# Optimization experiments

Measured on AMD Instinct MI355X. Metric: run time of the kernel, lower is better.

## Reference

```python
import jax, jax.numpy as jnp
import numpy as np

WINDOW = 512          # init window_size
OVERLAP = WINDOW // 4 # 128
FADE = OVERLAP // 2   # 64
ROPE_BASE = 10000.0


def _rope(x, pos):
    # x: (B,H,nw,W,D), pos: (nw,W) float
    D = x.shape[-1]
    inv_freq = 1.0 / (ROPE_BASE ** (jnp.arange(0, D, 2, dtype=jnp.float32) / D))
    ang = pos[..., None] * inv_freq                     # (nw,W,D/2)
    cos = jnp.concatenate([jnp.cos(ang), jnp.cos(ang)], -1)[None, None]  # (1,1,nw,W,D)
    sin = jnp.concatenate([jnp.sin(ang), jnp.sin(ang)], -1)[None, None]
    x1, x2 = x[..., : D // 2], x[..., D // 2 :]
    rot = jnp.concatenate([-x2, x1], -1)
    return x * cos + rot * sin


def setup_inputs() -> dict:
    key = jax.random.key(0)
    k1, k2, k3 = jax.random.split(key, 3)
    B, H, L, D = 2, 16, 8192, 64
    return {
        "query": jax.random.normal(k1, (B, H, L, D), jnp.float32),
        "key": jax.random.normal(k2, (B, H, L, D), jnp.float32),
        "value": jax.random.normal(k3, (B, H, L, D), jnp.float32),
        "position_ids": jnp.arange(L, dtype=jnp.int64),
    }


def reference(query, key, value, position_ids):
    B, H, L, D = query.shape
    nw = L // WINDOW
    qw = query.reshape(B, H, nw, WINDOW, D)
    kw = key.reshape(B, H, nw, WINDOW, D)
    vw = value.reshape(B, H, nw, WINDOW, D)
    pos = position_ids.reshape(nw, WINDOW).astype(jnp.float32)

    q = _rope(qw, pos)
    k = _rope(kw, pos)

    scores = jnp.einsum("bhnqd,bhnkd->bhnqk", q, k) / jnp.sqrt(jnp.float32(D))
    attn = jax.nn.softmax(scores, axis=-1)
    win_out = jnp.einsum("bhnqk,bhnkd->bhnqd", attn, vw)  # (B,H,nw,W,D)

    # overlap-fade blend weights per window (middle windows fade at edges;
    # first/last windows use full weight). out = win_out * w / (w + 1e-8).
    fade_in = jnp.linspace(0.0, 1.0, FADE)
    fade_out = jnp.linspace(1.0, 0.0, FADE)
    w_mid = jnp.concatenate([fade_in, jnp.ones(WINDOW - 2 * FADE), fade_out])
    w_edge = jnp.ones(WINDOW)
    idx = jnp.arange(nw)
    is_edge = (idx == 0) | (idx == nw - 1)
    w = jnp.where(is_edge[:, None], w_edge[None, :], w_mid[None, :])  # (nw,W)
    scale = (w / (w + 1e-8))[None, None, :, :, None]
    out = win_out * scale
    return out.reshape(B, H, L, D)
```

## Files before the change

kernel.cpp:

```cpp
#include <hip/hip_runtime.h>

typedef _Float16 half8 __attribute__((ext_vector_type(8)));
typedef _Float16 half4 __attribute__((ext_vector_type(4)));
typedef _Float16 half2v __attribute__((ext_vector_type(2)));
typedef float floatx4 __attribute__((ext_vector_type(4)));
typedef float floatx2 __attribute__((ext_vector_type(2)));

#define MFMA_F16 __builtin_amdgcn_mfma_f32_16x16x32_f16
#define FREQ (-0.41524101186092f)

__global__ __launch_bounds__(512, 4) void swa4(
    const float* __restrict__ Q, const float* __restrict__ K,
    const float* __restrict__ V, const int* __restrict__ pid,
    float* __restrict__ Out)
{
    __shared__ __align__(16) _Float16 lq[128 * 72];
    __shared__ __align__(16) _Float16 lk[2][32 * 64];
    __shared__ __align__(16) _Float16 lvt[2][64 * 32];
    __shared__ __align__(16) _Float16 lp[8][16 * 40];

    const int bid   = blockIdx.x;
    const int half_ = (bid >> 3) & 1;
    const int win   = (bid & 7) | ((bid >> 4) << 3);
    const int n = win & 15, bh = win >> 4;
    const long long winrow = (long long)bh * 8192 + n * 512;
    const long long qbase  = winrow + half_ * 256;
    const float* Qb = Q + qbase * 64;
    const float* Kb = K + winrow * 64;
    const float* Vb = V + winrow * 64;
    float* Ob = Out + qbase * 64;
    const int pidq = n * 512 + half_ * 256;
    const int pidk = n * 512;

    const int tid = threadIdx.x, lane = tid & 63, wv = tid >> 6;
    const int l15 = lane & 15, quad = (lane >> 4) & 3;
    const float CS = 0.125f * 1.44269504088896f;

    half8 qf[2][2];
    {
        const int rowl = tid >> 2;
        const int dq   = (tid & 3) * 8;
        float ifq[8];
        #pragma unroll
        for (int i = 0; i < 8; ++i) ifq[i] = __builtin_exp2f((float)(dq + i) * FREQ);
        for (int rnd = 0; rnd < 2; ++rnd) {
            const float* src = Qb + (rnd * 128 + rowl) * 64;
            float pos = (float)pid[pidq + rnd * 128 + rowl];
            float4 a0 = *(const float4*)(src + dq);
            float4 a1 = *(const float4*)(src + dq + 4);
            float4 b0 = *(const float4*)(src + 32 + dq);
            float4 b1 = *(const float4*)(src + 36 + dq);
            float lo[8] = {a0.x,a0.y,a0.z,a0.w,a1.x,a1.y,a1.z,a1.w};
            float hi[8] = {b0.x,b0.y,b0.z,b0.w,b1.x,b1.y,b1.z,b1.w};
            half8 wlo, whi;
            #pragma unroll
            for (int i = 0; i < 8; ++i) {
                float sn, cn;
                __sincosf(pos * ifq[i], &sn, &cn);
                wlo[i] = (_Float16)((lo[i] * cn - hi[i] * sn) * CS);
                whi[i] = (_Float16)((hi[i] * cn + lo[i] * sn) * CS);
            }
            if (rnd) __syncthreads();
            *(half8*)&lq[rowl * 72 + dq]      = wlo;
            *(half8*)&lq[rowl * 72 + 32 + dq] = whi;
            __syncthreads();
            if ((wv >> 2) == rnd) {
                const int rb = (wv & 3) * 32;
                #pragma unroll
                for (int rt = 0; rt < 2; ++rt) {
                    qf[rt][0] = *(const half8*)&lq[(rb + rt * 16 + l15) * 72 + quad * 8];
                    qf[rt][1] = *(const half8*)&lq[(rb + rt * 16 + l15) * 72 + 32 + quad * 8];
                }
            }
        }
    }

    floatx4 o[2][4], ol[2];
    #pragma unroll
    for (int rt = 0; rt < 2; ++rt) {
        ol[rt] = (floatx4){0.f, 0.f, 0.f, 0.f};
        #pragma unroll
        for (int vt = 0; vt < 4; ++vt) o[rt][vt] = (floatx4){0.f, 0.f, 0.f, 0.f};
    }
    half8 onesf;
    #pragma unroll
    for (int i = 0; i < 8; ++i) onesf[i] = (_Float16)1.0f;

    const int key = tid >> 4;
    const int pr  = tid & 15;
    const int dv  = tid & 63;
    const int grp = tid >> 6;
    float if2[2];
    #pragma unroll
    for (int i = 0; i < 2; ++i) if2[i] = __builtin_exp2f((float)(pr * 2 + i) * FREQ);
    const int klo_addr = key * 64 + (((pr >> 2) ^ (key & 7)) * 8) + (pr & 3) * 2;
    const int khi_addr = key * 64 + ((((pr >> 2) + 4) ^ (key & 7)) * 8) + (pr & 3) * 2;
    const int vst_addr = dv * 32 + (((grp >> 1) ^ ((dv >> 1) & 3)) * 8) + (grp & 1) * 4;
    const int ksw0 = (quad ^ (l15 & 7)) * 8;
    const int ksw1 = ((quad + 4) ^ (l15 & 7)) * 8;
    const int vsw  = (quad ^ ((l15 >> 1) & 3)) * 8;

    floatx2 ka  = *(const floatx2*)(Kb + key * 64 + pr * 2);
    floatx2 kb2 = *(const floatx2*)(Kb + key * 64 + 32 + pr * 2);
    float vr[4];
    #pragma unroll
    for (int i = 0; i < 4; ++i) vr[i] = Vb[(grp * 4 + i) * 64 + dv];
    int kp = pid[pidk + key];

    for (int kc = 0; kc < 16; ++kc) {
        const int cur = kc & 1;
        float kpos = (float)kp;
        half2v klo, khi;
        {
            float a[2] = {ka.x, ka.y};
            float b[2] = {kb2.x, kb2.y};
            #pragma unroll
            for (int i = 0; i < 2; ++i) {
                float sn, cn;
                __sincosf(kpos * if2[i], &sn, &cn);
                klo[i] = (_Float16)(a[i] * cn - b[i] * sn);
                khi[i] = (_Float16)(b[i] * cn + a[i] * sn);
            }
        }
        half4 vh;
        #pragma unroll
        for (int i = 0; i < 4; ++i) vh[i] = (_Float16)vr[i];

        *(half2v*)&lk[cur][klo_addr] = klo;
        *(half2v*)&lk[cur][khi_addr] = khi;
        *(half4*)&lvt[cur][vst_addr] = vh;
        __syncthreads();

        if (kc < 15) {
            const float* kn = Kb + (kc + 1) * 2048;
            const float* vn = Vb + (kc + 1) * 2048;
            ka  = *(const floatx2*)(kn + key * 64 + pr * 2);
            kb2 = *(const floatx2*)(kn + key * 64 + 32 + pr * 2);
            #pragma unroll
            for (int i = 0; i < 4; ++i) vr[i] = vn[(grp * 4 + i) * 64 + dv];
            kp = pid[pidk + (kc + 1) * 32 + key];
        }

        half8 kf00 = *(const half8*)&lk[cur][l15 * 64 + ksw0];
        half8 kf01 = *(const half8*)&lk[cur][l15 * 64 + ksw1];
        half8 kf10 = *(const half8*)&lk[cur][(16 + l15) * 64 + ksw0];
        half8 kf11 = *(const half8*)&lk[cur][(16 + l15) * 64 + ksw1];
        half8 vf[4];
        #pragma unroll
        for (int vt = 0; vt < 4; ++vt)
            vf[vt] = *(const half8*)&lvt[cur][(vt * 16 + l15) * 32 + vsw];

        #pragma unroll
        for (int rt = 0; rt < 2; ++rt) {
            floatx4 s0 = {0.f,0.f,0.f,0.f}, s1 = {0.f,0.f,0.f,0.f};
            s0 = MFMA_F16(qf[rt][0], kf00, s0, 0, 0, 0);
            s0 = MFMA_F16(qf[rt][1], kf01, s0, 0, 0, 0);
            s1 = MFMA_F16(qf[rt][0], kf10, s1, 0, 0, 0);
            s1 = MFMA_F16(qf[rt][1], kf11, s1, 0, 0, 0);

            #pragma unroll
            for (int r = 0; r < 4; ++r) {
                float p0 = __builtin_exp2f(s0[r]);
                float p1 = __builtin_exp2f(s1[r]);
                lp[wv][(quad * 4 + r) * 40 + l15]      = (_Float16)p0;
                lp[wv][(quad * 4 + r) * 40 + 16 + l15] = (_Float16)p1;
            }
            half8 pf = *(const half8*)&lp[wv][l15 * 40 + quad * 8];
            ol[rt] = MFMA_F16(pf, onesf, ol[rt], 0, 0, 0);
            #pragma unroll
            for (int vt = 0; vt < 4; ++vt)
                o[rt][vt] = MFMA_F16(pf, vf[vt], o[rt][vt], 0, 0, 0);
        }
    }

    #pragma unroll
    for (int rt = 0; rt < 2; ++rt) {
        #pragma unroll
        for (int r = 0; r < 4; ++r) {
            int rowl = wv * 32 + rt * 16 + quad * 4 + r;
            int j = half_ * 256 + rowl;
            float w;
            if (n == 0 || n == 15)  w = 1.0f;
            else if (j < 64)        w = (float)j * (1.0f / 63.0f);
            else if (j >= 448)      w = (float)(511 - j) * (1.0f / 63.0f);
            else                    w = 1.0f;
            float f = (w / (w + 1e-8f)) / ol[rt][r];
            #pragma unroll
            for (int vt = 0; vt < 4; ++vt)
                Ob[rowl * 64 + vt * 16 + l15] = o[rt][vt][r] * f;
        }
    }
}

extern "C" void kernel_launch(void* const* d_in, const int* in_sizes, int n_in,
                              void* d_out, int out_size, void* d_ws, size_t ws_size,
                              hipStream_t stream) {
    const float* q   = (const float*)d_in[0];
    const float* k   = (const float*)d_in[1];
    const float* v   = (const float*)d_in[2];
    const int*   pid = (const int*)d_in[3];
    float* out = (float*)d_out;
    (void)in_sizes; (void)n_in; (void)out_size; (void)d_ws; (void)ws_size;
    swa4<<<dim3(1024), dim3(512), 0, stream>>>(q, k, v, pid, out);
}
```

Baseline: 238.1 us.

## Compute transposed scores so P stays in registers, drop LDS P round-trip

```diff
diff --git a/kernel.cpp b/kernel.cpp
--- a/kernel.cpp
+++ b/kernel.cpp
@@ -9,7 +9,12 @@
 #define MFMA_F16 __builtin_amdgcn_mfma_f32_16x16x32_f16
 #define FREQ (-0.41524101186092f)
 
-__global__ __launch_bounds__(512, 4) void swa4(
+static __device__ __forceinline__ unsigned pack_f16(float a, float b) {
+    half2v h; h.x = (_Float16)a; h.y = (_Float16)b;
+    return __builtin_bit_cast(unsigned, h);
+}
+
+__global__ __launch_bounds__(512, 4) void swa6(
     const float* __restrict__ Q, const float* __restrict__ K,
     const float* __restrict__ V, const int* __restrict__ pid,
     float* __restrict__ Out)
@@ -17,7 +22,6 @@
     __shared__ __align__(16) _Float16 lq[128 * 72];
     __shared__ __align__(16) _Float16 lk[2][32 * 64];
     __shared__ __align__(16) _Float16 lvt[2][64 * 32];
-    __shared__ __align__(16) _Float16 lp[8][16 * 40];
 
     const int bid   = blockIdx.x;
     const int half_ = (bid >> 3) & 1;
@@ -95,7 +99,7 @@
     for (int i = 0; i < 2; ++i) if2[i] = __builtin_exp2f((float)(pr * 2 + i) * FREQ);
     const int klo_addr = key * 64 + (((pr >> 2) ^ (key & 7)) * 8) + (pr & 3) * 2;
     const int khi_addr = key * 64 + ((((pr >> 2) + 4) ^ (key & 7)) * 8) + (pr & 3) * 2;
-    const int vst_addr = dv * 32 + (((grp >> 1) ^ ((dv >> 1) & 3)) * 8) + (grp & 1) * 4;
+    const int vst_addr = dv * 32 + (((grp & 3) ^ ((dv >> 1) & 3)) * 8) + (grp >> 2) * 4;
     const int ksw0 = (quad ^ (l15 & 7)) * 8;
     const int ksw1 = ((quad + 4) ^ (l15 & 7)) * 8;
     const int vsw  = (quad ^ ((l15 >> 1) & 3)) * 8;
@@ -150,27 +154,28 @@
         for (int vt = 0; vt < 4; ++vt)
             vf[vt] = *(const half8*)&lvt[cur][(vt * 16 + l15) * 32 + vsw];
 
+        __builtin_amdgcn_s_setprio(1);
         #pragma unroll
         for (int rt = 0; rt < 2; ++rt) {
             floatx4 s0 = {0.f,0.f,0.f,0.f}, s1 = {0.f,0.f,0.f,0.f};
-            s0 = MFMA_F16(qf[rt][0], kf00, s0, 0, 0, 0);
-            s0 = MFMA_F16(qf[rt][1], kf01, s0, 0, 0, 0);
-            s1 = MFMA_F16(qf[rt][0], kf10, s1, 0, 0, 0);
-            s1 = MFMA_F16(qf[rt][1], kf11, s1, 0, 0, 0);
-
-            #pragma unroll
-            for (int r = 0; r < 4; ++r) {
-                float p0 = __builtin_exp2f(s0[r]);
-                float p1 = __builtin_exp2f(s1[r]);
-                lp[wv][(quad * 4 + r) * 40 + l15]      = (_Float16)p0;
-                lp[wv][(quad * 4 + r) * 40 + 16 + l15] = (_Float16)p1;
-            }
-            half8 pf = *(const half8*)&lp[wv][l15 * 40 + quad * 8];
+            s0 = MFMA_F16(kf00, qf[rt][0], s0, 0, 0, 0);
+            s0 = MFMA_F16(kf01, qf[rt][1], s0, 0, 0, 0);
+            s1 = MFMA_F16(kf10, qf[rt][0], s1, 0, 0, 0);
+            s1 = MFMA_F16(kf11, qf[rt][1], s1, 0, 0, 0);
+
+            union { unsigned u[4]; half8 h; } pfu;
+            pfu.u[0] = pack_f16(__builtin_exp2f(s0[0]), __builtin_exp2f(s0[1]));
+            pfu.u[1] = pack_f16(__builtin_exp2f(s0[2]), __builtin_exp2f(s0[3]));
+            pfu.u[2] = pack_f16(__builtin_exp2f(s1[0]), __builtin_exp2f(s1[1]));
+            pfu.u[3] = pack_f16(__builtin_exp2f(s1[2]), __builtin_exp2f(s1[3]));
+            half8 pf = pfu.h;
+
             ol[rt] = MFMA_F16(pf, onesf, ol[rt], 0, 0, 0);
             #pragma unroll
             for (int vt = 0; vt < 4; ++vt)
                 o[rt][vt] = MFMA_F16(pf, vf[vt], o[rt][vt], 0, 0, 0);
         }
+        __builtin_amdgcn_s_setprio(0);
     }
 
     #pragma unroll
@@ -201,5 +206,5 @@
     const int*   pid = (const int*)d_in[3];
     float* out = (float*)d_out;
     (void)in_sizes; (void)n_in; (void)out_size; (void)d_ws; (void)ws_size;
-    swa4<<<dim3(1024), dim3(512), 0, stream>>>(q, k, v, pid, out);
+    swa6<<<dim3(1024), dim3(512), 0, stream>>>(q, k, v, pid, out);
 }
```

Measured after the change: 234.5 us. No clear change (-1.5%).
